# Kernel optimization log

Measured on AMD Instinct MI355X. Metric: run time of the kernel, lower is better.

The kernel has to match this reference:

```python
import jax, jax.numpy as jnp
import numpy as np

DIM = 512
HEADS = 16
HEAD_DIM = DIM // HEADS
WH, WW = 7, 7
N = WH * WW
OUP = 512
SCALE = HEAD_DIM ** -0.5
NW = 64  # windows per image (mask leading dim)


def _relative_position_index():
    coords = np.stack(np.meshgrid(np.arange(WH), np.arange(WW), indexing='ij'))  # (2,Wh,Ww)
    flat = coords.reshape(2, -1)                           # (2, N)
    rel = flat[:, :, None] - flat[:, None, :]              # (2, N, N)
    rel = rel.transpose(1, 2, 0).astype(np.int64)          # (N, N, 2)
    rel[:, :, 0] += WH - 1
    rel[:, :, 1] += WW - 1
    rel[:, :, 0] *= 2 * WW - 1
    return jnp.asarray(rel.sum(-1))                        # (N, N) int

REL_IDX = _relative_position_index()


def setup_inputs() -> dict:
    key = jax.random.key(0)
    ks = jax.random.split(key, 8)
    B_ = 4096
    x = jax.random.normal(ks[0], (B_, N, DIM), dtype=jnp.float32)
    mask = jnp.zeros((NW, N, N), dtype=jnp.float32)
    qkv_w = jax.random.normal(ks[1], (3 * DIM, DIM), dtype=jnp.float32) * (DIM ** -0.5)
    qkv_b = jax.random.normal(ks[2], (3 * DIM,), dtype=jnp.float32) * 0.02
    table = jax.random.normal(ks[3], ((2 * WH - 1) * (2 * WW - 1), HEADS), dtype=jnp.float32) * 0.02
    proj_w = jax.random.normal(ks[4], (OUP, DIM), dtype=jnp.float32) * (DIM ** -0.5)
    proj_b = jax.random.normal(ks[5], (OUP,), dtype=jnp.float32) * 0.02
    return {"x": x, "mask": mask, "qkv_w": qkv_w, "qkv_b": qkv_b,
            "table": table, "proj_w": proj_w, "proj_b": proj_b}


def reference(x, mask, qkv_w, qkv_b, table, proj_w, proj_b):
    B_, n, c = x.shape
    qkv = x @ qkv_w.T + qkv_b                               # (B_, N, 3C)
    qkv = qkv.reshape(B_, n, 3, HEADS, HEAD_DIM).transpose(2, 0, 3, 1, 4)
    q, k, v = qkv[0], qkv[1], qkv[2]                        # (B_, H, N, hd)
    q = q * SCALE
    attn = jnp.einsum('bhnd,bhmd->bhnm', q, k)              # (B_, H, N, N)
    bias = table[REL_IDX]                                   # (N, N, H) gather
    attn = attn + bias.transpose(2, 0, 1)[None]             # add rel-pos bias
    nW = mask.shape[0]
    attn = attn.reshape(B_ // nW, nW, HEADS, n, n) + mask[None, :, None]
    attn = attn.reshape(B_, HEADS, n, n)
    attn = jax.nn.softmax(attn, axis=-1)
    out = jnp.einsum('bhnm,bhmd->bhnd', attn, v)            # (B_, H, N, hd)
    out = out.transpose(0, 2, 1, 3).reshape(B_, n, c)
    return out @ proj_w.T + proj_b
```

## Files before the change

### kernel.cpp

```cpp
#include <hip/hip_runtime.h>
#include <hip/hip_bf16.h>
#include <stdint.h>

#define DIMC 512
#define HEADS 16
#define HEAD_DIM 32
#define NTOK 49
#define SCALE 0.17677669529663687f
#define LOG2E 1.4426950408889634f
#define MTOK 200704

typedef unsigned short u16;
typedef short bf16x8 __attribute__((ext_vector_type(8)));
typedef float f32x4 __attribute__((ext_vector_type(4)));
typedef u16 u16x4 __attribute__((ext_vector_type(4)));
typedef u16 u16x8 __attribute__((ext_vector_type(8)));

#define MFMA16(a, b, c) __builtin_amdgcn_mfma_f32_16x16x32_bf16((a), (b), (c), 0, 0, 0)

__device__ __forceinline__ u16 f2bf(float f) {
  __hip_bfloat16 h = __float2bfloat16(f);
  u16 u;
  __builtin_memcpy(&u, &h, 2);
  return u;
}

__device__ __forceinline__ float bf2f(u16 u) {
  const uint32_t b = ((uint32_t)u) << 16;
  float f;
  __builtin_memcpy(&f, &b, 4);
  return f;
}

__device__ __forceinline__ void gld16(const void* g, void* l) {
  __builtin_amdgcn_global_load_lds(
      (const __attribute__((address_space(1))) uint32_t*)g,
      (__attribute__((address_space(3))) uint32_t*)l, 16, 0, 0);
}

__global__ void cvt_f32_bf16(const float* __restrict__ in, u16* __restrict__ out, int n) {
  const int stride = gridDim.x * blockDim.x;
  for (int i = blockIdx.x * blockDim.x + threadIdx.x; i * 8 < n; i += stride) {
    const float4 v0 = ((const float4*)(in + i * 8))[0];
    const float4 v1 = ((const float4*)(in + i * 8))[1];
    u16x8 r;
    r[0] = f2bf(v0.x); r[1] = f2bf(v0.y); r[2] = f2bf(v0.z); r[3] = f2bf(v0.w);
    r[4] = f2bf(v1.x); r[5] = f2bf(v1.y); r[6] = f2bf(v1.z); r[7] = f2bf(v1.w);
    *(u16x8*)(out + i * 8) = r;
  }
}

__global__ void biasmask_kernel(const float* __restrict__ table, const float* __restrict__ mask,
                                u16* __restrict__ bm) {
  const int wm = blockIdx.x >> 4;
  const int h  = blockIdx.x & 15;
  for (int e = threadIdx.x; e < 4096; e += 256) {
    const int r = e & 3, lane = (e >> 2) & 63, fj = (e >> 8) & 3, fi = e >> 10;
    const int qrow = fi * 16 + (lane & 15);
    const int kcol = fj * 16 + (lane >> 4) * 4 + r;
    float v;
    if (qrow < NTOK && kcol < NTOK) {
      const int yi = qrow / 7, xi = qrow % 7, yj = kcol / 7, xj = kcol % 7;
      const int idx = (yi - yj + 6) * 13 + (xi - xj + 6);
      v = (table[idx * HEADS + h] + mask[wm * (NTOK * NTOK) + qrow * NTOK + kcol]) * LOG2E;
    } else {
      v = -1e30f;
    }
    bm[(size_t)blockIdx.x * 4096 + e] = f2bf(v);
  }
}

template<bool OUT_BF16, bool HEADMAJOR>
__global__ void gemm_bf16(const u16* __restrict__ Ap, const u16* __restrict__ Bp,
                          const float* __restrict__ bias, void* __restrict__ Cp,
                          int M, int N, int K, int nxt) {
  __shared__ u16 As[128 * 64];
  __shared__ u16 Bs[128 * 64];
  const int t = threadIdx.x;
  const int lane = t & 63;
  const int q = gridDim.x >> 3;
  const int lin = blockIdx.x;
  const int l = (lin & 7) * q + (lin >> 3);
  const int bm0 = (l / nxt) * 128;
  const int bn0 = (l % nxt) * 128;
  const int wv = t >> 6, wr = wv >> 1, wc = wv & 1;
  const int lr = lane & 15, lg = lane >> 4;

  f32x4 acc[4][4] = {};

  int soff[4];
#pragma unroll
  for (int k = 0; k < 4; ++k) {
    const int c = t + 256 * k;
    const int row = c >> 3, sub = c & 7;
    soff[k] = ((sub ^ (row & 7)) * 8);
  }

  const int nK = K >> 6;
  for (int kt = 0; kt < nK; ++kt) {
    const int k0 = kt << 6;
    __syncthreads();
#pragma unroll
    for (int k = 0; k < 4; ++k) {
      const int c = t + 256 * k;
      const int row = c >> 3;
      gld16(Ap + (size_t)(bm0 + row) * K + k0 + soff[k], As + c * 8);
      gld16(Bp + (size_t)(bn0 + row) * K + k0 + soff[k], Bs + c * 8);
    }
    __syncthreads();

#pragma unroll
    for (int kk = 0; kk < 2; ++kk) {
      bf16x8 af[4], bfr[4];
#pragma unroll
      for (int i = 0; i < 4; ++i) {
        const int row = wr * 64 + i * 16 + lr;
        af[i] = *(const bf16x8*)&As[row * 64 + (((kk * 4 + lg) ^ (row & 7)) << 3)];
      }
#pragma unroll
      for (int j = 0; j < 4; ++j) {
        const int row = wc * 64 + j * 16 + lr;
        bfr[j] = *(const bf16x8*)&Bs[row * 64 + (((kk * 4 + lg) ^ (row & 7)) << 3)];
      }
#pragma unroll
      for (int i = 0; i < 4; ++i)
#pragma unroll
        for (int j = 0; j < 4; ++j)
          acc[i][j] = MFMA16(af[i], bfr[j], acc[i][j]);
    }
  }

#pragma unroll
  for (int j = 0; j < 4; ++j) {
    const int col = bn0 + wc * 64 + j * 16 + lr;
    const float bv = bias[col];
    const int p = col >> 9, hh = (col & 511) >> 5, d = col & 31;
    const float sc = (HEADMAJOR && p == 0) ? SCALE * LOG2E : 1.0f;
#pragma unroll
    for (int i = 0; i < 4; ++i) {
      const int row0 = bm0 + wr * 64 + i * 16 + lg * 4;
#pragma unroll
      for (int r = 0; r < 4; ++r) {
        const float val = (acc[i][j][r] + bv) * sc;
        if (HEADMAJOR) {
          ((u16*)Cp)[((size_t)hh * MTOK + row0 + r) * 96 + p * 32 + d] = f2bf(val);
        } else if (OUT_BF16) {
          ((u16*)Cp)[(size_t)(row0 + r) * N + col] = f2bf(val);
        } else {
          ((float*)Cp)[(size_t)(row0 + r) * N + col] = val;
        }
      }
    }
  }
}

__launch_bounds__(256, 4)
__global__ void attn_win(const u16* __restrict__ qkv, const u16* __restrict__ bmfrag,
                         u16* __restrict__ aout) {
  __shared__ u16 P[4][64 * 72];
  const int t = threadIdx.x, lane = t & 63, wv = t >> 6;
  const int lr = lane & 15, lg = lane >> 4;
  const int w = blockIdx.x >> 2;
  const int h = ((blockIdx.x & 3) << 2) + wv;
  const size_t baseh = ((size_t)h * MTOK + (size_t)w * NTOK) * 96;

  const u16* bmp = bmfrag + (((size_t)(w & 63) * 16 + h) << 12);
  f32x4 s[4][4];
#pragma unroll
  for (int i = 0; i < 4; ++i)
#pragma unroll
    for (int j = 0; j < 4; ++j) {
      const u16x4 b4 = *(const u16x4*)&bmp[((i * 4 + j) * 64 + lane) * 4];
#pragma unroll
      for (int r = 0; r < 4; ++r) s[i][j][r] = bf2f(b4[r]);
    }

  const bf16x8 zf = {};
  bf16x8 qf[4], kf[4];
#pragma unroll
  for (int i = 0; i < 4; ++i) {
    const int row = i * 16 + lr;
    const size_t roff = baseh + (size_t)row * 96 + lg * 8;
    qf[i] = (row < NTOK) ? *(const bf16x8*)&qkv[roff] : zf;
    kf[i] = (row < NTOK) ? *(const bf16x8*)&qkv[roff + 32] : zf;
  }

  __builtin_amdgcn_s_setprio(1);
#pragma unroll
  for (int i = 0; i < 4; ++i)
#pragma unroll
    for (int j = 0; j < 4; ++j)
      s[i][j] = MFMA16(kf[j], qf[i], s[i][j]);
  __builtin_amdgcn_s_setprio(0);

  u16* Pw = &P[wv][0];
#pragma unroll
  for (int i = 0; i < 4; ++i)
#pragma unroll
    for (int j = 0; j < 4; ++j) {
      u16x4 pk;
#pragma unroll
      for (int r = 0; r < 4; ++r)
        pk[r] = f2bf(__builtin_amdgcn_exp2f(s[i][j][r]));
      *(u16x4*)&Pw[(i * 16 + lr) * 72 + j * 16 + lg * 4] = pk;
    }

  bf16x8 vf[2][2];
#pragma unroll
  for (int ks = 0; ks < 2; ++ks)
#pragma unroll
    for (int dn = 0; dn < 2; ++dn)
#pragma unroll
      for (int e = 0; e < 8; ++e) {
        int kk = ks * 32 + lg * 8 + e;
        kk = kk < NTOK ? kk : 0;
        vf[ks][dn][e] = (short)qkv[baseh + (size_t)kk * 96 + 64 + dn * 16 + lr];
      }

  bf16x8 ones;
#pragma unroll
  for (int e = 0; e < 8; ++e) ones[e] = (short)0x3F80;
  f32x4 o[4][2] = {};
  f32x4 osum[4] = {};
#pragma unroll
  for (int ks = 0; ks < 2; ++ks) {
    __builtin_amdgcn_s_setprio(1);
#pragma unroll
    for (int i = 0; i < 4; ++i) {
      const bf16x8 pa = *(const bf16x8*)&Pw[(i * 16 + lr) * 72 + ks * 32 + lg * 8];
#pragma unroll
      for (int dn = 0; dn < 2; ++dn)
        o[i][dn] = MFMA16(pa, vf[ks][dn], o[i][dn]);
      osum[i] = MFMA16(pa, ones, osum[i]);
    }
    __builtin_amdgcn_s_setprio(0);
  }

#pragma unroll
  for (int i = 0; i < 4; ++i)
#pragma unroll
    for (int r = 0; r < 4; ++r) {
      const int row = i * 16 + lg * 4 + r;
      if (row < NTOK) {
        const float rinv = __builtin_amdgcn_rcpf(osum[i][r]);
        const size_t ob = ((size_t)w * NTOK + row) * DIMC + h * HEAD_DIM;
#pragma unroll
        for (int dn = 0; dn < 2; ++dn)
          aout[ob + dn * 16 + lr] = f2bf(o[i][dn][r] * rinv);
      }
    }
}

extern "C" void kernel_launch(void* const* d_in, const int* in_sizes, int n_in,
                              void* d_out, int out_size, void* d_ws, size_t ws_size,
                              hipStream_t stream) {
  const float* x      = (const float*)d_in[0];
  const float* mask   = (const float*)d_in[1];
  const float* qkv_w  = (const float*)d_in[2];
  const float* qkv_b  = (const float*)d_in[3];
  const float* table  = (const float*)d_in[4];
  const float* proj_w = (const float*)d_in[5];
  const float* proj_b = (const float*)d_in[6];
  float* out = (float*)d_out;

  const int M = MTOK;

  char* ws = (char*)d_ws;
  u16*   qkv_bf   = (u16*)ws;
  u16*   wqkv_bf  = (u16*)(ws + 616562688ull);
  u16*   wproj_bf = (u16*)(ws + 618135552ull);
  u16*   biasmask = (u16*)(ws + 618659840ull);
  u16*   x_bf     = (u16*)(ws + 627048448ull);
  u16*   attn_bf  = x_bf;

  cvt_f32_bf16<<<768, 256, 0, stream>>>(qkv_w, wqkv_bf, 1536 * 512);
  cvt_f32_bf16<<<256, 256, 0, stream>>>(proj_w, wproj_bf, 512 * 512);
  biasmask_kernel<<<1024, 256, 0, stream>>>(table, mask, biasmask);
  cvt_f32_bf16<<<1792, 256, 0, stream>>>(x, x_bf, M * DIMC);

  gemm_bf16<true, true><<<1568 * 12, 256, 0, stream>>>(
      x_bf, wqkv_bf, qkv_b, qkv_bf, M, 1536, 512, 12);

  attn_win<<<4096 * 4, 256, 0, stream>>>(qkv_bf, biasmask, attn_bf);

  gemm_bf16<false, false><<<1568 * 4, 256, 0, stream>>>(
      attn_bf, wproj_bf, proj_b, out, M, 512, 512, 4);
}
```

Baseline: 962.4 us.

## Store V transposed from QKV GEMM to enable vector loads in attention

The QKV GEMM epilogue now writes Q and K into a 64-wide head-major buffer and V into a separate transposed buffer (head, dim, token) padded by 64 tokens. The attention kernel then loads V fragments as 8-element vectors instead of 8 scalar strided gathers per fragment, and issues those loads earlier, before the score MFMAs. In exchange, the V stores in the GEMM epilogue become strided across tokens, which may hurt write coalescing. Padded tokens beyond the window read neighbouring-window values, but those keys get zero probability through the -1e30 bias.

```diff
diff --git a/kernel.cpp b/kernel.cpp
--- a/kernel.cpp
+++ b/kernel.cpp
@@ -9,6 +9,7 @@
 #define SCALE 0.17677669529663687f
 #define LOG2E 1.4426950408889634f
 #define MTOK 200704
+#define MTOKP 200768
 
 typedef unsigned short u16;
 typedef short bf16x8 __attribute__((ext_vector_type(8)));
@@ -73,6 +74,7 @@
 template<bool OUT_BF16, bool HEADMAJOR>
 __global__ void gemm_bf16(const u16* __restrict__ Ap, const u16* __restrict__ Bp,
                           const float* __restrict__ bias, void* __restrict__ Cp,
+                          u16* __restrict__ CpV,
                           int M, int N, int K, int nxt) {
   __shared__ u16 As[128 * 64];
   __shared__ u16 Bs[128 * 64];
@@ -143,7 +145,10 @@
       for (int r = 0; r < 4; ++r) {
         const float val = (acc[i][j][r] + bv) * sc;
         if (HEADMAJOR) {
-          ((u16*)Cp)[((size_t)hh * MTOK + row0 + r) * 96 + p * 32 + d] = f2bf(val);
+          if (p < 2)
+            ((u16*)Cp)[((size_t)hh * MTOK + row0 + r) * 64 + p * 32 + d] = f2bf(val);
+          else
+            CpV[((size_t)hh * 32 + d) * MTOKP + row0 + r] = f2bf(val);
         } else if (OUT_BF16) {
           ((u16*)Cp)[(size_t)(row0 + r) * N + col] = f2bf(val);
         } else {
@@ -155,14 +160,14 @@
 }
 
 __launch_bounds__(256, 4)
-__global__ void attn_win(const u16* __restrict__ qkv, const u16* __restrict__ bmfrag,
-                         u16* __restrict__ aout) {
+__global__ void attn_win(const u16* __restrict__ qk, const u16* __restrict__ vT,
+                         const u16* __restrict__ bmfrag, u16* __restrict__ aout) {
   __shared__ u16 P[4][64 * 72];
   const int t = threadIdx.x, lane = t & 63, wv = t >> 6;
   const int lr = lane & 15, lg = lane >> 4;
   const int w = blockIdx.x >> 2;
   const int h = ((blockIdx.x & 3) << 2) + wv;
-  const size_t baseh = ((size_t)h * MTOK + (size_t)w * NTOK) * 96;
+  const size_t baseqk = ((size_t)h * MTOK + (size_t)w * NTOK) * 64;
 
   const u16* bmp = bmfrag + (((size_t)(w & 63) * 16 + h) << 12);
   f32x4 s[4][4];
@@ -180,10 +185,18 @@
 #pragma unroll
   for (int i = 0; i < 4; ++i) {
     const int row = i * 16 + lr;
-    const size_t roff = baseh + (size_t)row * 96 + lg * 8;
-    qf[i] = (row < NTOK) ? *(const bf16x8*)&qkv[roff] : zf;
-    kf[i] = (row < NTOK) ? *(const bf16x8*)&qkv[roff + 32] : zf;
-  }
+    const size_t roff = baseqk + (size_t)row * 64 + lg * 8;
+    qf[i] = (row < NTOK) ? *(const bf16x8*)&qk[roff] : zf;
+    kf[i] = (row < NTOK) ? *(const bf16x8*)&qk[roff + 32] : zf;
+  }
+
+  bf16x8 vf[2][2];
+#pragma unroll
+  for (int ks = 0; ks < 2; ++ks)
+#pragma unroll
+    for (int dn = 0; dn < 2; ++dn)
+      vf[ks][dn] = *(const bf16x8*)&vT[((size_t)h * 32 + dn * 16 + lr) * MTOKP +
+                                       (size_t)w * NTOK + ks * 32 + lg * 8];
 
   __builtin_amdgcn_s_setprio(1);
 #pragma unroll
@@ -204,18 +217,6 @@
         pk[r] = f2bf(__builtin_amdgcn_exp2f(s[i][j][r]));
       *(u16x4*)&Pw[(i * 16 + lr) * 72 + j * 16 + lg * 4] = pk;
     }
-
-  bf16x8 vf[2][2];
-#pragma unroll
-  for (int ks = 0; ks < 2; ++ks)
-#pragma unroll
-    for (int dn = 0; dn < 2; ++dn)
-#pragma unroll
-      for (int e = 0; e < 8; ++e) {
-        int kk = ks * 32 + lg * 8 + e;
-        kk = kk < NTOK ? kk : 0;
-        vf[ks][dn][e] = (short)qkv[baseh + (size_t)kk * 96 + 64 + dn * 16 + lr];
-      }
 
   bf16x8 ones;
 #pragma unroll
@@ -266,11 +267,12 @@
   const int M = MTOK;
 
   char* ws = (char*)d_ws;
-  u16*   qkv_bf   = (u16*)ws;
-  u16*   wqkv_bf  = (u16*)(ws + 616562688ull);
-  u16*   wproj_bf = (u16*)(ws + 618135552ull);
-  u16*   biasmask = (u16*)(ws + 618659840ull);
-  u16*   x_bf     = (u16*)(ws + 627048448ull);
+  u16*   qk_bf    = (u16*)ws;
+  u16*   vT_bf    = (u16*)(ws + 411041792ull);
+  u16*   wqkv_bf  = (u16*)(ws + 616628224ull);
+  u16*   wproj_bf = (u16*)(ws + 618201088ull);
+  u16*   biasmask = (u16*)(ws + 618725376ull);
+  u16*   x_bf     = (u16*)(ws + 627113984ull);
   u16*   attn_bf  = x_bf;
 
   cvt_f32_bf16<<<768, 256, 0, stream>>>(qkv_w, wqkv_bf, 1536 * 512);
@@ -279,10 +281,10 @@
   cvt_f32_bf16<<<1792, 256, 0, stream>>>(x, x_bf, M * DIMC);
 
   gemm_bf16<true, true><<<1568 * 12, 256, 0, stream>>>(
-      x_bf, wqkv_bf, qkv_b, qkv_bf, M, 1536, 512, 12);
-
-  attn_win<<<4096 * 4, 256, 0, stream>>>(qkv_bf, biasmask, attn_bf);
+      x_bf, wqkv_bf, qkv_b, qk_bf, vT_bf, M, 1536, 512, 12);
+
+  attn_win<<<4096 * 4, 256, 0, stream>>>(qk_bf, vT_bf, biasmask, attn_bf);
 
   gemm_bf16<false, false><<<1568 * 4, 256, 0, stream>>>(
-      attn_bf, wproj_bf, proj_b, out, M, 512, 512, 4);
-}
+      attn_bf, wproj_bf, proj_b, out, nullptr, M, 512, 512, 4);
+}
```

Measured after the change: 1.133 ms. 1.18x slower.
